# Kernel tuning notes

Hardware: AMD Instinct MI355X
Metric: run time of the kernel (lower is better)

## Reference

```python
import jax, jax.numpy as jnp
import numpy as np
from jax import lax

B, S, H = 2, 1024, 1024   # batch, seq, hidden_size
I = 512                   # moe_intermediate_size
E = 16                    # num_experts
TOP_K = 8                 # num_experts_per_tok


def setup_inputs() -> dict:
    key = jax.random.key(0)
    ks = jax.random.split(key, 5)
    scale_h = 1.0 / np.sqrt(H)
    scale_i = 1.0 / np.sqrt(I)
    return {
        "hidden_states": jax.random.normal(ks[0], (B, S, H), dtype=jnp.float32),
        "gate_w": jax.random.normal(ks[1], (H, E), dtype=jnp.float32) * scale_h,   # router
        "w_gate": jax.random.normal(ks[2], (E, H, I), dtype=jnp.float32) * scale_h,
        "w_up":   jax.random.normal(ks[3], (E, H, I), dtype=jnp.float32) * scale_h,
        "w_down": jax.random.normal(ks[4], (E, I, H), dtype=jnp.float32) * scale_i,
    }


def reference(hidden_states, gate_w, w_gate, w_up, w_down):
    b, s, h = hidden_states.shape
    x = hidden_states.reshape(-1, h)                      # [T, H]
    T = x.shape[0]

    router_logits = x @ gate_w                            # [T, E]
    probs = jax.nn.softmax(router_logits.astype(jnp.float32), axis=-1)
    top_w, top_i = lax.top_k(probs, TOP_K)                # [T, K]
    top_w = top_w / jnp.sum(top_w, axis=-1, keepdims=True)  # norm_topk_prob
    top_w = top_w.astype(x.dtype)

    # Dense per-token combine weights [T, E]; zero for unselected experts
    combine = jnp.zeros((T, E), dtype=x.dtype)
    combine = combine.at[jnp.arange(T)[:, None], top_i].add(top_w)

    # Scan over experts: masked gated-MLP, weighted accumulate (exact math;
    # unselected tokens contribute with weight 0, matching index_add scatter).
    def expert_step(acc, ws):
        wg, wu, wd, ce = ws                               # ce: [T] combine weights
        hmid = jax.nn.silu(x @ wg) * (x @ wu)             # [T, I]
        return acc + (hmid @ wd) * ce[:, None], None

    out, _ = lax.scan(expert_step, jnp.zeros_like(x),
                      (w_gate, w_up, w_down, combine.T))
    return out.reshape(b, s, h), router_logits
```

## Files before the change

### kernel.cpp

```cpp
#include <hip/hip_runtime.h>

typedef __attribute__((ext_vector_type(8))) short bf16x8;
typedef __attribute__((ext_vector_type(4))) float f32x4;
typedef __attribute__((ext_vector_type(4))) unsigned short u16x4;


static __device__ __forceinline__ unsigned short f2bfu(float f) {
  union { float f; unsigned u; } v; v.f = f;
  return (unsigned short)((v.u + 0x7fffu + ((v.u >> 16) & 1u)) >> 16);
}

static __device__ __forceinline__ float bfu2f(unsigned short u) {
  union { unsigned u; float f; } v; v.u = ((unsigned)u) << 16; return v.f;
}

static __device__ __forceinline__ void gload_lds16(const void* g, void* l) {
  __builtin_amdgcn_global_load_lds(
      (const __attribute__((address_space(1))) unsigned int*)g,
      (__attribute__((address_space(3))) unsigned int*)l, 16, 0, 0);
}

__global__ __launch_bounds__(256) void k_transall(const float* __restrict__ wga,
                                                  const float* __restrict__ wup,
                                                  const float* __restrict__ wdo,
                                                  unsigned short* __restrict__ wgt,
                                                  unsigned short* __restrict__ wut,
                                                  unsigned short* __restrict__ wdt2) {
  __shared__ float tile[64][65];
  const int z = blockIdx.z;
  const float* src;
  unsigned short* dst;
  int R, C, ostride;
  if (z < 16)      { src = wga + (size_t)z * 524288; dst = wgt + (size_t)z * 524288; R = 1024; C = 512; ostride = 1024; }
  else if (z < 32) { src = wup + (size_t)(z-16) * 524288; dst = wut + (size_t)(z-16) * 524288; R = 1024; C = 512; ostride = 1024; }
  else             { src = wdo + (size_t)(z-32) * 524288; dst = wdt2 + (size_t)(z-32) * 524288; R = 512; C = 1024; ostride = 512; }
  int c0 = blockIdx.x * 64, r0 = blockIdx.y * 64;
  if (c0 >= C || r0 >= R) return;
  int cc = (threadIdx.x & 15) * 4, rr = threadIdx.x >> 4;
#pragma unroll
  for (int i = 0; i < 4; ++i) {
    float4 v = *(const float4*)(src + (size_t)(r0 + rr + i * 16) * C + c0 + cc);
    tile[rr + i * 16][cc + 0] = v.x; tile[rr + i * 16][cc + 1] = v.y;
    tile[rr + i * 16][cc + 2] = v.z; tile[rr + i * 16][cc + 3] = v.w;
  }
  __syncthreads();
#pragma unroll
  for (int i = 0; i < 4; ++i) {
    int oc = rr + i * 16;
    u16x4 o = { f2bfu(tile[cc + 0][oc]), f2bfu(tile[cc + 1][oc]),
                f2bfu(tile[cc + 2][oc]), f2bfu(tile[cc + 3][oc]) };
    *(u16x4*)(dst + (size_t)(c0 + oc) * ostride + r0 + cc) = o;
  }
}

__global__ __launch_bounds__(64) void k_router(const float* __restrict__ x,
                                               const float* __restrict__ gw,
                                               float* __restrict__ combine,
                                               float* __restrict__ logits,
                                               unsigned short* __restrict__ xb) {
  int t = blockIdx.x;
  int lane = threadIdx.x;
  const float* xr = x + (size_t)t * 1024;
  unsigned short* xbr = xb + (size_t)t * 1024;
  float acc[16];
#pragma unroll
  for (int e = 0; e < 16; ++e) acc[e] = 0.f;
  for (int h = lane; h < 1024; h += 64) {
    float xv = xr[h];
    xbr[h] = f2bfu(xv);
    const float4* gr = (const float4*)(gw + (size_t)h * 16);
#pragma unroll
    for (int q = 0; q < 4; ++q) {
      float4 g4 = gr[q];
      acc[q * 4 + 0] += xv * g4.x;
      acc[q * 4 + 1] += xv * g4.y;
      acc[q * 4 + 2] += xv * g4.z;
      acc[q * 4 + 3] += xv * g4.w;
    }
  }
#pragma unroll
  for (int e = 0; e < 16; ++e) {
#pragma unroll
    for (int off = 32; off > 0; off >>= 1)
      acc[e] += __shfl_xor(acc[e], off);
  }
  if (lane < 16) logits[(size_t)t * 16 + lane] = acc[lane];

  float m = acc[0];
#pragma unroll
  for (int e = 1; e < 16; ++e) m = fmaxf(m, acc[e]);
  unsigned sel = 0u;
  for (int k = 0; k < 8; ++k) {
    float best = -3.4e38f; int bi = 0;
#pragma unroll
    for (int e = 0; e < 16; ++e)
      if (!((sel >> e) & 1u) && acc[e] > best) { best = acc[e]; bi = e; }
    sel |= 1u << bi;
  }
  float s = 0.f;
#pragma unroll
  for (int e = 0; e < 16; ++e)
    if ((sel >> e) & 1u) s += expf(acc[e] - m);
  float inv = 1.f / s;
  if (lane < 16)
    combine[(size_t)t * 16 + lane] = ((sel >> lane) & 1u) ? expf(acc[lane] - m) * inv : 0.f;
}

__global__ __launch_bounds__(256) void k_scan(const float* __restrict__ combine,
                                              unsigned short* __restrict__ idxlist,
                                              int* __restrict__ tokslot,
                                              int* __restrict__ counts) {
  __shared__ int wsum[4];
  const int e = blockIdx.x;
  const int tid = threadIdx.x;
  const int lane = tid & 63, w = tid >> 6;
  const int t0 = tid * 8;
  int flags = 0, cnt = 0;
#pragma unroll
  for (int j = 0; j < 8; ++j) {
    float c = combine[(size_t)(t0 + j) * 16 + e];
    if (c != 0.f) { flags |= 1 << j; ++cnt; }
  }
  int scan = cnt;
#pragma unroll
  for (int off = 1; off < 64; off <<= 1) {
    int v = __shfl_up(scan, off);
    if (lane >= off) scan += v;
  }
  if (lane == 63) wsum[w] = scan;
  __syncthreads();
  int base = 0;
  for (int i = 0; i < w; ++i) base += wsum[i];
  int pos = base + scan - cnt;
  for (int j = 0; j < 8; ++j) {
    if ((flags >> j) & 1) {
      idxlist[e * 2048 + pos] = (unsigned short)(t0 + j);
      tokslot[(t0 + j) * 16 + e] = pos;
      ++pos;
    } else {
      tokslot[(t0 + j) * 16 + e] = -1;
    }
  }
  if (tid == 255) counts[e] = base + scan;
}

__global__ __launch_bounds__(256) void k_gateup(const unsigned short* __restrict__ xb,
                                                const unsigned short* __restrict__ wgt,
                                                const unsigned short* __restrict__ wut,
                                                const unsigned short* __restrict__ idxlist,
                                                const int* __restrict__ counts,
                                                unsigned short* __restrict__ midp) {
  const int lb = (int)(blockIdx.x & 7) * 256 + (int)(blockIdx.x >> 3);
  const int p = lb & 255, it = lb >> 8;
  int e = -1, mt = 0, Ne = 0, gb = 0, acc = 0;
#pragma unroll
  for (int i = 0; i < 16; ++i) {
    int c = counts[i];
    int nt = (c + 127) >> 7;
    if (e < 0) {
      if (p < acc + nt) { e = i; mt = p - acc; Ne = c; }
      else gb += c;
    }
    acc += nt;
  }
  if (e < 0) return;
  const int m0 = mt * 128;
  const int i0 = it * 64;

  __shared__ alignas(16) char lds[49152];

  const int tid = threadIdx.x;
  const int lane = tid & 63;
  const int w = tid >> 6;
  const int wm = (w >> 1) * 64;
  const int wn = (w & 1) * 32;

  const int crow = lane >> 2;
  const int slog = (lane & 3) ^ ((crow >> 1) & 3);

  const unsigned short* wge = wgt + (size_t)e * (512 * 1024);
  const unsigned short* wue = wut + (size_t)e * (512 * 1024);

  const unsigned short* gsrc[4];
  int loff[4];
#pragma unroll
  for (int q = 0; q < 4; ++q) {
    int c = w * 4 + q;
    loff[q] = c * 1024;
    if (c < 8) {
      int slot = m0 + c * 16 + crow;
      slot = slot < Ne ? slot : Ne - 1;
      gsrc[q] = xb + (size_t)idxlist[e * 2048 + slot] * 1024 + slog * 8;
    } else if (c < 12) {
      gsrc[q] = wge + (size_t)(i0 + (c - 8) * 16 + crow) * 1024 + slog * 8;
    } else {
      gsrc[q] = wue + (size_t)(i0 + (c - 12) * 16 + crow) * 1024 + slog * 8;
    }
  }

  auto stage = [&](int buf, int k0) {
    char* base = lds + buf * 16384;
#pragma unroll
    for (int q = 0; q < 4; ++q)
      gload_lds16(gsrc[q] + k0, base + loff[q]);
  };

  const int r0 = lane & 15;
  const int gp16 = ((lane >> 4) ^ ((r0 >> 1) & 3)) << 4;
  const int aoff  = ((wm + r0) << 6) + gp16;
  const int bgoff = 8192  + ((wn + r0) << 6) + gp16;
  const int buoff = 12288 + ((wn + r0) << 6) + gp16;

  f32x4 accg[4][2], accu[4][2];
#pragma unroll
  for (int fm = 0; fm < 4; ++fm)
#pragma unroll
    for (int fn = 0; fn < 2; ++fn) {
      accg[fm][fn] = f32x4{0.f, 0.f, 0.f, 0.f};
      accu[fm][fn] = f32x4{0.f, 0.f, 0.f, 0.f};
    }

  stage(0, 0);
  stage(1, 32);
  int cur = 0;
  for (int t = 0; t < 32; ++t) {
    if (t == 31) asm volatile("s_waitcnt vmcnt(0)" ::: "memory");
    else         asm volatile("s_waitcnt vmcnt(4)" ::: "memory");
    __builtin_amdgcn_s_barrier();
    const char* base = lds + cur * 16384;
    bf16x8 a[4], bg[2], bu[2];
#pragma unroll
    for (int fm = 0; fm < 4; ++fm) a[fm] = *(const bf16x8*)(base + aoff + fm * 1024);
#pragma unroll
    for (int fn = 0; fn < 2; ++fn) {
      bg[fn] = *(const bf16x8*)(base + bgoff + fn * 1024);
      bu[fn] = *(const bf16x8*)(base + buoff + fn * 1024);
    }
    asm volatile("s_waitcnt lgkmcnt(0)" ::: "memory");
    __builtin_amdgcn_sched_barrier(0);
    if (t + 2 < 32) {
      int nb = cur + 2; if (nb >= 3) nb -= 3;
      stage(nb, (t + 2) * 32);
    }
    __builtin_amdgcn_s_setprio(1);
#pragma unroll
    for (int fm = 0; fm < 4; ++fm)
#pragma unroll
      for (int fn = 0; fn < 2; ++fn) {
        accg[fm][fn] = __builtin_amdgcn_mfma_f32_16x16x32_bf16(a[fm], bg[fn], accg[fm][fn], 0, 0, 0);
        accu[fm][fn] = __builtin_amdgcn_mfma_f32_16x16x32_bf16(a[fm], bu[fn], accu[fm][fn], 0, 0, 0);
      }
    __builtin_amdgcn_s_setprio(0);
    if (++cur == 3) cur = 0;
  }

  const int gq = lane >> 4;
#pragma unroll
  for (int fm = 0; fm < 4; ++fm) {
#pragma unroll
    for (int jj = 0; jj < 4; ++jj) {
      int slot = m0 + wm + fm * 16 + gq * 4 + jj;
      if (slot >= Ne) continue;
#pragma unroll
      for (int fn = 0; fn < 2; ++fn) {
        float gv = accg[fm][fn][jj];
        float uv = accu[fm][fn][jj];
        float mv = gv / (1.f + __expf(-gv)) * uv;
        midp[(size_t)(gb + slot) * 512 + i0 + wn + fn * 16 + r0] = f2bfu(mv);
      }
    }
  }
}

__global__ __launch_bounds__(512) void k_down(const unsigned short* __restrict__ midp,
                                              const unsigned short* __restrict__ wdt2,
                                              const int* __restrict__ counts,
                                              unsigned short* __restrict__ dpk) {
  const int lb = (int)(blockIdx.x & 7) * 256 + (int)(blockIdx.x >> 3);
  const int mt = lb & 7, ht = (lb >> 3) & 15, e = lb >> 7;
  int Ne = counts[e], gb = 0;
#pragma unroll
  for (int i = 0; i < 16; ++i) { int c = counts[i]; if (i < e) gb += c; }
  const int m0 = mt * 256;
  if (m0 >= Ne) return;
  const int h0 = ht * 64;

  __shared__ alignas(16) char lds[61440];

  const int tid = threadIdx.x;
  const int lane = tid & 63;
  const int w = tid >> 6;
  const int wm = (w >> 1) * 64;
  const int wn = (w & 1) * 32;

  const int crow = lane >> 2;
  const int slog = (lane & 3) ^ ((crow >> 1) & 3);

  const unsigned short* bsrc = wdt2 + (size_t)e * (512 * 1024);

  const unsigned short* gsrcA[2];
  int loffA[2];
#pragma unroll
  for (int q = 0; q < 2; ++q) {
    int c = q * 8 + w;
    loffA[q] = c * 1024;
    int slot = m0 + c * 16 + crow;
    slot = slot < Ne ? slot : Ne - 1;
    gsrcA[q] = midp + (size_t)(gb + slot) * 512 + slog * 8;
  }
  const unsigned short* gsrcB = nullptr;
  int loffB = 0;
  if (w >= 4) {
    loffB = 16384 + (w - 4) * 1024;
    gsrcB = bsrc + (size_t)(h0 + (w - 4) * 16 + crow) * 512 + slog * 8;
  }

  auto stage = [&](int buf, int k0) {
    char* base = lds + buf * 20480;
#pragma unroll
    for (int q = 0; q < 2; ++q)
      gload_lds16(gsrcA[q] + k0, base + loffA[q]);
    if (gsrcB) gload_lds16(gsrcB + k0, base + loffB);
  };

  const int r0 = lane & 15;
  const int gp16 = ((lane >> 4) ^ ((r0 >> 1) & 3)) << 4;
  const int aoff = ((wm + r0) << 6) + gp16;
  const int boff = 16384 + ((wn + r0) << 6) + gp16;

  f32x4 acc[4][2];
#pragma unroll
  for (int fm = 0; fm < 4; ++fm)
#pragma unroll
    for (int fn = 0; fn < 2; ++fn) acc[fm][fn] = f32x4{0.f, 0.f, 0.f, 0.f};

  stage(0, 0);
  stage(1, 32);
  int cur = 0;
  for (int t = 0; t < 16; ++t) {
    if (t == 15)       asm volatile("s_waitcnt vmcnt(0)" ::: "memory");
    else if (w >= 4)   asm volatile("s_waitcnt vmcnt(3)" ::: "memory");
    else               asm volatile("s_waitcnt vmcnt(2)" ::: "memory");
    __builtin_amdgcn_s_barrier();
    const char* base = lds + cur * 20480;
    bf16x8 a[4], b[2];
#pragma unroll
    for (int fm = 0; fm < 4; ++fm) a[fm] = *(const bf16x8*)(base + aoff + fm * 1024);
#pragma unroll
    for (int fn = 0; fn < 2; ++fn) b[fn] = *(const bf16x8*)(base + boff + fn * 1024);
    asm volatile("s_waitcnt lgkmcnt(0)" ::: "memory");
    __builtin_amdgcn_sched_barrier(0);
    if (t + 2 < 16) {
      int nb = cur + 2; if (nb >= 3) nb -= 3;
      stage(nb, (t + 2) * 32);
    }
    __builtin_amdgcn_s_setprio(1);
#pragma unroll
    for (int fm = 0; fm < 4; ++fm)
#pragma unroll
      for (int fn = 0; fn < 2; ++fn)
        acc[fm][fn] = __builtin_amdgcn_mfma_f32_16x16x32_bf16(a[fm], b[fn], acc[fm][fn], 0, 0, 0);
    __builtin_amdgcn_s_setprio(0);
    if (++cur == 3) cur = 0;
  }

  const int gq = lane >> 4;
#pragma unroll
  for (int fm = 0; fm < 4; ++fm)
#pragma unroll
    for (int jj = 0; jj < 4; ++jj) {
      int slot = m0 + wm + fm * 16 + gq * 4 + jj;
      if (slot >= Ne) continue;
#pragma unroll
      for (int fn = 0; fn < 2; ++fn)
        dpk[(size_t)(gb + slot) * 1024 + h0 + wn + fn * 16 + r0] = f2bfu(acc[fm][fn][jj]);
    }
}

__global__ __launch_bounds__(128) void k_combine(const unsigned short* __restrict__ dpk,
                                                 const int* __restrict__ tokslot,
                                                 const int* __restrict__ counts,
                                                 const float* __restrict__ combine,
                                                 float* __restrict__ out) {
  __shared__ int gsl[16];
  __shared__ float cws[16];
  const int t = blockIdx.x;
  const int tid = threadIdx.x;
  if (tid < 16) {
    int eb = 0;
    for (int i = 0; i < tid; ++i) eb += counts[i];
    int sl = tokslot[t * 16 + tid];
    gsl[tid] = (sl >= 0) ? eb + sl : -1;
    cws[tid] = combine[(size_t)t * 16 + tid];
  }
  __syncthreads();
  float av[8];
#pragma unroll
  for (int j = 0; j < 8; ++j) av[j] = 0.f;
#pragma unroll
  for (int e = 0; e < 16; ++e) {
    int g = gsl[e];
    if (g < 0) continue;
    float cw = cws[e];
    bf16x8 v = *(const bf16x8*)(dpk + (size_t)g * 1024 + tid * 8);
#pragma unroll
    for (int j = 0; j < 8; ++j) av[j] += cw * bfu2f((unsigned short)v[j]);
  }
  float4 lo = { av[0], av[1], av[2], av[3] };
  float4 hi = { av[4], av[5], av[6], av[7] };
  float4* op = (float4*)(out + (size_t)t * 1024 + tid * 8);
  op[0] = lo;
  op[1] = hi;
}

extern "C" void kernel_launch(void* const* d_in, const int* in_sizes, int n_in,
                              void* d_out, int out_size, void* d_ws, size_t ws_size,
                              hipStream_t stream) {
  const float* x   = (const float*)d_in[0];
  const float* gw  = (const float*)d_in[1];
  const float* wga = (const float*)d_in[2];
  const float* wup = (const float*)d_in[3];
  const float* wdo = (const float*)d_in[4];
  float* out = (float*)d_out;
  float* logits = out + (size_t)2048 * 1024;

  char* ws = (char*)d_ws;
  unsigned short* xb   = (unsigned short*)(ws + 0);
  unsigned short* wgt  = (unsigned short*)(ws + 4194304);
  unsigned short* wut  = (unsigned short*)(ws + 20971520);
  unsigned short* wdt2 = (unsigned short*)(ws + 37748736);
  unsigned short* midp = (unsigned short*)(ws + 54525952);
  float* combine       = (float*)(ws + 71303168);
  int* tokslot         = (int*)(ws + 71434240);
  unsigned short* idxl = (unsigned short*)(ws + 71565312);
  int* counts          = (int*)(ws + 71630848);
  unsigned short* dpk  = (unsigned short*)(ws + 4194304);

  k_transall<<<dim3(16, 16, 48), 256, 0, stream>>>(wga, wup, wdo, wgt, wut, wdt2);
  k_router<<<2048, 64, 0, stream>>>(x, gw, combine, logits, xb);
  k_scan<<<16, 256, 0, stream>>>(combine, idxl, tokslot, counts);
  k_gateup<<<2048, 256, 0, stream>>>(xb, wgt, wut, idxl, counts, midp);
  k_down<<<2048, 512, 0, stream>>>(midp, wdt2, counts, dpk);
  k_combine<<<2048, 128, 0, stream>>>(dpk, tokslot, counts, combine, out);
}
```

Baseline: 141.4 us.

## Merge weight transpose with router and enlarge gate-up and down GEMM tiles

```diff
diff --git a/kernel.cpp b/kernel.cpp
--- a/kernel.cpp
+++ b/kernel.cpp
@@ -20,46 +20,47 @@
       (__attribute__((address_space(3))) unsigned int*)l, 16, 0, 0);
 }
 
-__global__ __launch_bounds__(256) void k_transall(const float* __restrict__ wga,
-                                                  const float* __restrict__ wup,
-                                                  const float* __restrict__ wdo,
-                                                  unsigned short* __restrict__ wgt,
-                                                  unsigned short* __restrict__ wut,
-                                                  unsigned short* __restrict__ wdt2) {
-  __shared__ float tile[64][65];
-  const int z = blockIdx.z;
-  const float* src;
-  unsigned short* dst;
-  int R, C, ostride;
-  if (z < 16)      { src = wga + (size_t)z * 524288; dst = wgt + (size_t)z * 524288; R = 1024; C = 512; ostride = 1024; }
-  else if (z < 32) { src = wup + (size_t)(z-16) * 524288; dst = wut + (size_t)(z-16) * 524288; R = 1024; C = 512; ostride = 1024; }
-  else             { src = wdo + (size_t)(z-32) * 524288; dst = wdt2 + (size_t)(z-32) * 524288; R = 512; C = 1024; ostride = 512; }
-  int c0 = blockIdx.x * 64, r0 = blockIdx.y * 64;
-  if (c0 >= C || r0 >= R) return;
-  int cc = (threadIdx.x & 15) * 4, rr = threadIdx.x >> 4;
-#pragma unroll
-  for (int i = 0; i < 4; ++i) {
-    float4 v = *(const float4*)(src + (size_t)(r0 + rr + i * 16) * C + c0 + cc);
-    tile[rr + i * 16][cc + 0] = v.x; tile[rr + i * 16][cc + 1] = v.y;
-    tile[rr + i * 16][cc + 2] = v.z; tile[rr + i * 16][cc + 3] = v.w;
-  }
-  __syncthreads();
-#pragma unroll
-  for (int i = 0; i < 4; ++i) {
-    int oc = rr + i * 16;
-    u16x4 o = { f2bfu(tile[cc + 0][oc]), f2bfu(tile[cc + 1][oc]),
-                f2bfu(tile[cc + 2][oc]), f2bfu(tile[cc + 3][oc]) };
-    *(u16x4*)(dst + (size_t)(c0 + oc) * ostride + r0 + cc) = o;
-  }
-}
-
-__global__ __launch_bounds__(64) void k_router(const float* __restrict__ x,
-                                               const float* __restrict__ gw,
-                                               float* __restrict__ combine,
-                                               float* __restrict__ logits,
-                                               unsigned short* __restrict__ xb) {
-  int t = blockIdx.x;
-  int lane = threadIdx.x;
+__global__ __launch_bounds__(256) void k_prep(const float* __restrict__ wga,
+                                              const float* __restrict__ wup,
+                                              const float* __restrict__ wdo,
+                                              unsigned short* __restrict__ wgt,
+                                              unsigned short* __restrict__ wut,
+                                              unsigned short* __restrict__ wdt2,
+                                              const float* __restrict__ x,
+                                              const float* __restrict__ gw,
+                                              float* __restrict__ combine,
+                                              float* __restrict__ logits,
+                                              unsigned short* __restrict__ xb) {
+  const int bid = blockIdx.x;
+  if (bid < 6144) {
+    __shared__ float tile[64][65];
+    const int zz = bid >> 7;
+    const int rem = bid & 127;
+    const float* src;
+    unsigned short* dst;
+    int C, ostride, c0, r0;
+    if (zz < 16)      { src = wga + (size_t)zz * 524288; dst = wgt + (size_t)zz * 524288; C = 512; ostride = 1024; c0 = (rem & 7) * 64; r0 = (rem >> 3) * 64; }
+    else if (zz < 32) { src = wup + (size_t)(zz-16) * 524288; dst = wut + (size_t)(zz-16) * 524288; C = 512; ostride = 1024; c0 = (rem & 7) * 64; r0 = (rem >> 3) * 64; }
+    else              { src = wdo + (size_t)(zz-32) * 524288; dst = wdt2 + (size_t)(zz-32) * 524288; C = 1024; ostride = 512; c0 = (rem & 15) * 64; r0 = (rem >> 4) * 64; }
+    int cc = (threadIdx.x & 15) * 4, rr = threadIdx.x >> 4;
+#pragma unroll
+    for (int i = 0; i < 4; ++i) {
+      float4 v = *(const float4*)(src + (size_t)(r0 + rr + i * 16) * C + c0 + cc);
+      tile[rr + i * 16][cc + 0] = v.x; tile[rr + i * 16][cc + 1] = v.y;
+      tile[rr + i * 16][cc + 2] = v.z; tile[rr + i * 16][cc + 3] = v.w;
+    }
+    __syncthreads();
+#pragma unroll
+    for (int i = 0; i < 4; ++i) {
+      int oc = rr + i * 16;
+      u16x4 o = { f2bfu(tile[cc + 0][oc]), f2bfu(tile[cc + 1][oc]),
+                  f2bfu(tile[cc + 2][oc]), f2bfu(tile[cc + 3][oc]) };
+      *(u16x4*)(dst + (size_t)(c0 + oc) * ostride + r0 + cc) = o;
+    }
+    return;
+  }
+  const int t = (bid - 6144) * 4 + (threadIdx.x >> 6);
+  const int lane = threadIdx.x & 63;
   const float* xr = x + (size_t)t * 1024;
   unsigned short* xbr = xb + (size_t)t * 1024;
   float acc[16];
@@ -144,13 +145,13 @@
   if (tid == 255) counts[e] = base + scan;
 }
 
-__global__ __launch_bounds__(256) void k_gateup(const unsigned short* __restrict__ xb,
-                                                const unsigned short* __restrict__ wgt,
-                                                const unsigned short* __restrict__ wut,
-                                                const unsigned short* __restrict__ idxlist,
-                                                const int* __restrict__ counts,
-                                                unsigned short* __restrict__ midp) {
-  const int lb = (int)(blockIdx.x & 7) * 256 + (int)(blockIdx.x >> 3);
+__global__ __launch_bounds__(256, 2) void k_gateup(const unsigned short* __restrict__ xb,
+                                                   const unsigned short* __restrict__ wgt,
+                                                   const unsigned short* __restrict__ wut,
+                                                   const unsigned short* __restrict__ idxlist,
+                                                   const int* __restrict__ counts,
+                                                   unsigned short* __restrict__ midp) {
+  const int lb = (int)(blockIdx.x & 7) * 128 + (int)(blockIdx.x >> 3);
   const int p = lb & 255, it = lb >> 8;
   int e = -1, mt = 0, Ne = 0, gb = 0, acc = 0;
 #pragma unroll
@@ -165,15 +166,15 @@
   }
   if (e < 0) return;
   const int m0 = mt * 128;
-  const int i0 = it * 64;
-
-  __shared__ alignas(16) char lds[49152];
+  const int i0 = it * 128;
+
+  __shared__ alignas(16) char lds[73728];
 
   const int tid = threadIdx.x;
   const int lane = tid & 63;
   const int w = tid >> 6;
   const int wm = (w >> 1) * 64;
-  const int wn = (w & 1) * 32;
+  const int wn = (w & 1) * 64;
 
   const int crow = lane >> 2;
   const int slog = (lane & 3) ^ ((crow >> 1) & 3);
@@ -181,27 +182,27 @@
   const unsigned short* wge = wgt + (size_t)e * (512 * 1024);
   const unsigned short* wue = wut + (size_t)e * (512 * 1024);
 
-  const unsigned short* gsrc[4];
-  int loff[4];
-#pragma unroll
-  for (int q = 0; q < 4; ++q) {
-    int c = w * 4 + q;
+  const unsigned short* gsrc[6];
+  int loff[6];
+#pragma unroll
+  for (int q = 0; q < 6; ++q) {
+    int c = w * 6 + q;
     loff[q] = c * 1024;
     if (c < 8) {
       int slot = m0 + c * 16 + crow;
       slot = slot < Ne ? slot : Ne - 1;
       gsrc[q] = xb + (size_t)idxlist[e * 2048 + slot] * 1024 + slog * 8;
-    } else if (c < 12) {
+    } else if (c < 16) {
       gsrc[q] = wge + (size_t)(i0 + (c - 8) * 16 + crow) * 1024 + slog * 8;
     } else {
-      gsrc[q] = wue + (size_t)(i0 + (c - 12) * 16 + crow) * 1024 + slog * 8;
+      gsrc[q] = wue + (size_t)(i0 + (c - 16) * 16 + crow) * 1024 + slog * 8;
     }
   }
 
   auto stage = [&](int buf, int k0) {
-    char* base = lds + buf * 16384;
-#pragma unroll
-    for (int q = 0; q < 4; ++q)
+    char* base = lds + buf * 24576;
+#pragma unroll
+    for (int q = 0; q < 6; ++q)
       gload_lds16(gsrc[q] + k0, base + loff[q]);
   };
 
@@ -209,13 +210,13 @@
   const int gp16 = ((lane >> 4) ^ ((r0 >> 1) & 3)) << 4;
   const int aoff  = ((wm + r0) << 6) + gp16;
   const int bgoff = 8192  + ((wn + r0) << 6) + gp16;
-  const int buoff = 12288 + ((wn + r0) << 6) + gp16;
-
-  f32x4 accg[4][2], accu[4][2];
+  const int buoff = 16384 + ((wn + r0) << 6) + gp16;
+
+  f32x4 accg[4][4], accu[4][4];
 #pragma unroll
   for (int fm = 0; fm < 4; ++fm)
 #pragma unroll
-    for (int fn = 0; fn < 2; ++fn) {
+    for (int fn = 0; fn < 4; ++fn) {
       accg[fm][fn] = f32x4{0.f, 0.f, 0.f, 0.f};
       accu[fm][fn] = f32x4{0.f, 0.f, 0.f, 0.f};
     }
@@ -225,14 +226,14 @@
   int cur = 0;
   for (int t = 0; t < 32; ++t) {
     if (t == 31) asm volatile("s_waitcnt vmcnt(0)" ::: "memory");
-    else         asm volatile("s_waitcnt vmcnt(4)" ::: "memory");
+    else         asm volatile("s_waitcnt vmcnt(6)" ::: "memory");
     __builtin_amdgcn_s_barrier();
-    const char* base = lds + cur * 16384;
-    bf16x8 a[4], bg[2], bu[2];
+    const char* base = lds + cur * 24576;
+    bf16x8 a[4], bg[4], bu[4];
 #pragma unroll
     for (int fm = 0; fm < 4; ++fm) a[fm] = *(const bf16x8*)(base + aoff + fm * 1024);
 #pragma unroll
-    for (int fn = 0; fn < 2; ++fn) {
+    for (int fn = 0; fn < 4; ++fn) {
       bg[fn] = *(const bf16x8*)(base + bgoff + fn * 1024);
       bu[fn] = *(const bf16x8*)(base + buoff + fn * 1024);
     }
@@ -246,7 +247,7 @@
 #pragma unroll
     for (int fm = 0; fm < 4; ++fm)
 #pragma unroll
-      for (int fn = 0; fn < 2; ++fn) {
+      for (int fn = 0; fn < 4; ++fn) {
         accg[fm][fn] = __builtin_amdgcn_mfma_f32_16x16x32_bf16(a[fm], bg[fn], accg[fm][fn], 0, 0, 0);
         accu[fm][fn] = __builtin_amdgcn_mfma_f32_16x16x32_bf16(a[fm], bu[fn], accu[fm][fn], 0, 0, 0);
       }
@@ -262,7 +263,7 @@
       int slot = m0 + wm + fm * 16 + gq * 4 + jj;
       if (slot >= Ne) continue;
 #pragma unroll
-      for (int fn = 0; fn < 2; ++fn) {
+      for (int fn = 0; fn < 4; ++fn) {
         float gv = accg[fm][fn][jj];
         float uv = accu[fm][fn][jj];
         float mv = gv / (1.f + __expf(-gv)) * uv;
@@ -272,55 +273,52 @@
   }
 }
 
-__global__ __launch_bounds__(512) void k_down(const unsigned short* __restrict__ midp,
-                                              const unsigned short* __restrict__ wdt2,
-                                              const int* __restrict__ counts,
-                                              unsigned short* __restrict__ dpk) {
-  const int lb = (int)(blockIdx.x & 7) * 256 + (int)(blockIdx.x >> 3);
-  const int mt = lb & 7, ht = (lb >> 3) & 15, e = lb >> 7;
+__global__ __launch_bounds__(512, 4) void k_down(const unsigned short* __restrict__ midp,
+                                                 const unsigned short* __restrict__ wdt2,
+                                                 const int* __restrict__ counts,
+                                                 unsigned short* __restrict__ dpk) {
+  const int lb = (int)(blockIdx.x & 7) * 128 + (int)(blockIdx.x >> 3);
+  const int mt = lb & 7, ht = (lb >> 3) & 7, e = lb >> 6;
   int Ne = counts[e], gb = 0;
 #pragma unroll
   for (int i = 0; i < 16; ++i) { int c = counts[i]; if (i < e) gb += c; }
   const int m0 = mt * 256;
   if (m0 >= Ne) return;
-  const int h0 = ht * 64;
-
-  __shared__ alignas(16) char lds[61440];
+  const int h0 = ht * 128;
+
+  __shared__ alignas(16) char lds[73728];
 
   const int tid = threadIdx.x;
   const int lane = tid & 63;
   const int w = tid >> 6;
-  const int wm = (w >> 1) * 64;
-  const int wn = (w & 1) * 32;
+  const int wm = (w & 3) * 64;
+  const int wn = (w >> 2) * 64;
 
   const int crow = lane >> 2;
   const int slog = (lane & 3) ^ ((crow >> 1) & 3);
 
   const unsigned short* bsrc = wdt2 + (size_t)e * (512 * 1024);
 
-  const unsigned short* gsrcA[2];
-  int loffA[2];
-#pragma unroll
-  for (int q = 0; q < 2; ++q) {
-    int c = q * 8 + w;
-    loffA[q] = c * 1024;
-    int slot = m0 + c * 16 + crow;
-    slot = slot < Ne ? slot : Ne - 1;
-    gsrcA[q] = midp + (size_t)(gb + slot) * 512 + slog * 8;
-  }
-  const unsigned short* gsrcB = nullptr;
-  int loffB = 0;
-  if (w >= 4) {
-    loffB = 16384 + (w - 4) * 1024;
-    gsrcB = bsrc + (size_t)(h0 + (w - 4) * 16 + crow) * 512 + slog * 8;
+  const unsigned short* gsrc[3];
+  int loff[3];
+#pragma unroll
+  for (int q = 0; q < 3; ++q) {
+    int c = w * 3 + q;
+    loff[q] = c * 1024;
+    if (c < 16) {
+      int slot = m0 + c * 16 + crow;
+      slot = slot < Ne ? slot : Ne - 1;
+      gsrc[q] = midp + (size_t)(gb + slot) * 512 + slog * 8;
+    } else {
+      gsrc[q] = bsrc + (size_t)(h0 + (c - 16) * 16 + crow) * 512 + slog * 8;
+    }
   }
 
   auto stage = [&](int buf, int k0) {
-    char* base = lds + buf * 20480;
-#pragma unroll
-    for (int q = 0; q < 2; ++q)
-      gload_lds16(gsrcA[q] + k0, base + loffA[q]);
-    if (gsrcB) gload_lds16(gsrcB + k0, base + loffB);
+    char* base = lds + buf * 24576;
+#pragma unroll
+    for (int q = 0; q < 3; ++q)
+      gload_lds16(gsrc[q] + k0, base + loff[q]);
   };
 
   const int r0 = lane & 15;
@@ -328,26 +326,25 @@
   const int aoff = ((wm + r0) << 6) + gp16;
   const int boff = 16384 + ((wn + r0) << 6) + gp16;
 
-  f32x4 acc[4][2];
+  f32x4 acc[4][4];
 #pragma unroll
   for (int fm = 0; fm < 4; ++fm)
 #pragma unroll
-    for (int fn = 0; fn < 2; ++fn) acc[fm][fn] = f32x4{0.f, 0.f, 0.f, 0.f};
+    for (int fn = 0; fn < 4; ++fn) acc[fm][fn] = f32x4{0.f, 0.f, 0.f, 0.f};
 
   stage(0, 0);
   stage(1, 32);
   int cur = 0;
   for (int t = 0; t < 16; ++t) {
-    if (t == 15)       asm volatile("s_waitcnt vmcnt(0)" ::: "memory");
-    else if (w >= 4)   asm volatile("s_waitcnt vmcnt(3)" ::: "memory");
-    else               asm volatile("s_waitcnt vmcnt(2)" ::: "memory");
+    if (t == 15) asm volatile("s_waitcnt vmcnt(0)" ::: "memory");
+    else         asm volatile("s_waitcnt vmcnt(3)" ::: "memory");
     __builtin_amdgcn_s_barrier();
-    const char* base = lds + cur * 20480;
-    bf16x8 a[4], b[2];
+    const char* base = lds + cur * 24576;
+    bf16x8 a[4], b[4];
 #pragma unroll
     for (int fm = 0; fm < 4; ++fm) a[fm] = *(const bf16x8*)(base + aoff + fm * 1024);
 #pragma unroll
-    for (int fn = 0; fn < 2; ++fn) b[fn] = *(const bf16x8*)(base + boff + fn * 1024);
+    for (int fn = 0; fn < 4; ++fn) b[fn] = *(const bf16x8*)(base + boff + fn * 1024);
     asm volatile("s_waitcnt lgkmcnt(0)" ::: "memory");
     __builtin_amdgcn_sched_barrier(0);
     if (t + 2 < 16) {
@@ -358,7 +355,7 @@
 #pragma unroll
     for (int fm = 0; fm < 4; ++fm)
 #pragma unroll
-      for (int fn = 0; fn < 2; ++fn)
+      for (int fn = 0; fn < 4; ++fn)
         acc[fm][fn] = __builtin_amdgcn_mfma_f32_16x16x32_bf16(a[fm], b[fn], acc[fm][fn], 0, 0, 0);
     __builtin_amdgcn_s_setprio(0);
     if (++cur == 3) cur = 0;
@@ -372,7 +369,7 @@
       int slot = m0 + wm + fm * 16 + gq * 4 + jj;
       if (slot >= Ne) continue;
 #pragma unroll
-      for (int fn = 0; fn < 2; ++fn)
+      for (int fn = 0; fn < 4; ++fn)
         dpk[(size_t)(gb + slot) * 1024 + h0 + wn + fn * 16 + r0] = f2bfu(acc[fm][fn][jj]);
     }
 }
@@ -436,10 +433,9 @@
   int* counts          = (int*)(ws + 71630848);
   unsigned short* dpk  = (unsigned short*)(ws + 4194304);
 
-  k_transall<<<dim3(16, 16, 48), 256, 0, stream>>>(wga, wup, wdo, wgt, wut, wdt2);
-  k_router<<<2048, 64, 0, stream>>>(x, gw, combine, logits, xb);
+  k_prep<<<6656, 256, 0, stream>>>(wga, wup, wdo, wgt, wut, wdt2, x, gw, combine, logits, xb);
   k_scan<<<16, 256, 0, stream>>>(combine, idxl, tokslot, counts);
-  k_gateup<<<2048, 256, 0, stream>>>(xb, wgt, wut, idxl, counts, midp);
-  k_down<<<2048, 512, 0, stream>>>(midp, wdt2, counts, dpk);
+  k_gateup<<<1024, 256, 0, stream>>>(xb, wgt, wut, idxl, counts, midp);
+  k_down<<<1024, 512, 0, stream>>>(midp, wdt2, counts, dpk);
   k_combine<<<2048, 128, 0, stream>>>(dpk, tokslot, counts, combine, out);
 }
```

Measured after the change: 154.5 us. 9.3% more time.
